# Kernel tuning notes

Hardware: AMD Instinct MI355X
Metric: run time of the kernel (lower is better)

## Reference

```python
import jax, jax.numpy as jnp
import numpy as np

B, N, D_IN, D_OUT = 64, 307, 64, 64
ALPHA = 0.2  # LeakyReLU negative slope
NEG_INF = -9e15


def _build_adj(n, seed=0):
    # Mimic the module's constant adjacency buffer structure:
    # 2n x 2n, bottom-right = A, top-left = A, top-right = I, bottom-left = 0.
    rng = np.random.RandomState(seed)
    A = (rng.rand(n, n) < 0.05).astype(np.float32)
    np.fill_diagonal(A, 1.0)
    full = np.zeros((2 * n, 2 * n), dtype=np.float32)
    full[n:, n:] = A
    full[:n, :n] = A
    full[:n, n:] = np.eye(n, dtype=np.float32)
    return jnp.asarray(full)


def setup_inputs() -> dict:
    key = jax.random.key(0)
    k1, k2, k3, k4 = jax.random.split(key, 4)
    h = jax.random.normal(k1, (B, N, D_IN), dtype=jnp.float32)
    ht = jax.random.normal(k2, (B, N, D_IN), dtype=jnp.float32)
    # xavier_uniform-ish params
    bw = 1.414 * np.sqrt(6.0 / (D_IN + D_OUT))
    W = jax.random.uniform(k3, (D_IN, D_OUT), dtype=jnp.float32, minval=-bw, maxval=bw)
    ba = 1.414 * np.sqrt(6.0 / (2 * D_OUT + 1))
    a = jax.random.uniform(k4, (2 * D_OUT, 1), dtype=jnp.float32, minval=-ba, maxval=ba)
    adj = _build_adj(N)
    return {"h": h, "ht": ht, "W": W, "a": a, "adj": adj}


def reference(h, ht, W, a, adj):
    n = N
    x = jnp.concatenate([ht, h], axis=1)          # [b, 2n, d_in]
    Wh = jnp.einsum('bni,io->bno', x, W)          # [b, 2n, d_out]
    Wh1 = Wh @ a[:D_OUT]                          # [b, 2n, 1]
    Wh2 = Wh @ a[D_OUT:]                          # [b, 2n, 1]
    e = jax.nn.leaky_relu(Wh1 + jnp.swapaxes(Wh2, 1, 2), negative_slope=ALPHA)  # [b,2n,2n]
    att = jnp.where(adj > 0, e, NEG_INF)
    att = jax.nn.softmax(att, axis=1)             # NOTE: softmax over dim=1 as in source
    # dropout is identity in eval mode (training=False)
    h_prime = jnp.einsum('bnm,bmo->bno', att, Wh)  # [b, 2n, d_out]
    h_prime = jnp.concatenate([h_prime[:, :n], h_prime[:, n:]], axis=-1)  # [b, n, 2*d_out]
    return jax.nn.elu(h_prime)
```

## Files before the change

### kernel.cpp

```cpp
#include <hip/hip_runtime.h>
#include <hip/hip_bf16.h>
#include <math.h>

#define NB   64
#define NN   307
#define MM   614
#define DD   64
#define CAP  64
#define LRA  0.2f
#define WHB  39
#define NTASK (NB * NN)

__device__ __forceinline__ float wave_sum(float v) {
  #pragma unroll
  for (int m = 32; m >= 1; m >>= 1) v += __shfl_xor(v, m);
  return v;
}
__device__ __forceinline__ float lrelu(float v) { return v > 0.f ? v : LRA * v; }

__global__ __launch_bounds__(256) void k_prep(const float* __restrict__ h,
    const float* __restrict__ ht, const float* __restrict__ W,
    const float* __restrict__ a, const float* __restrict__ adj,
    int* __restrict__ arow_cnt, int* __restrict__ arow_idx,
    int* __restrict__ acol_cnt, int* __restrict__ acol_idx,
    float* __restrict__ Wh, float* __restrict__ Wh1, float* __restrict__ Wh2) {
  int tid = threadIdx.x;
  int bid = blockIdx.x;

  if (bid < 2 * NN) {
    __shared__ int cnt;
    if (tid == 0) cnt = 0;
    __syncthreads();
    if (bid < NN) {
      int r = bid;
      for (int j = tid; j < NN; j += 256)
        if (adj[(size_t)r * MM + j] > 0.f)
          arow_idx[r * CAP + atomicAdd(&cnt, 1)] = j;
      __syncthreads();
      if (tid == 0) arow_cnt[r] = cnt;
    } else {
      int c = bid - NN;
      for (int i = tid; i < NN; i += 256)
        if (adj[(size_t)i * MM + c] > 0.f)
          acol_idx[c * CAP + atomicAdd(&cnt, 1)] = i;
      __syncthreads();
      if (tid == 0) acol_cnt[c] = cnt;
    }
    return;
  }

  __shared__ float Wl[DD * DD];
  __shared__ float xst[4][DD][4];
  #pragma unroll
  for (int k = 0; k < 16; k++) Wl[tid + k * 256] = W[tid + k * 256];

  int lane = tid & 63;
  int wv   = __builtin_amdgcn_readfirstlane(tid >> 6);
  int blk  = bid - 2 * NN;
  int b    = blk / WHB;
  int r0   = (blk % WHB) * 16 + wv * 4;

  const float* xp[4];
  bool valid[4];
  #pragma unroll
  for (int j = 0; j < 4; j++) {
    int r = r0 + j;
    valid[j] = (r < MM);
    int rc = valid[j] ? r : 0;
    xp[j] = (rc < NN) ? (ht + ((size_t)b * NN + rc) * DD)
                      : (h  + ((size_t)b * NN + (rc - NN)) * DD);
  }
  int jr = lane & 3, el = lane >> 2;
  #pragma unroll
  for (int t = 0; t < 4; t++) {
    float v = xp[jr][t * 16 + el];
    xst[wv][t * 16 + el][jr] = v;
  }
  __syncthreads();

  float a1 = a[lane], a2 = a[64 + lane];
  float acc0 = 0.f, acc1 = 0.f, acc2 = 0.f, acc3 = 0.f;
  #pragma unroll
  for (int i = 0; i < 64; i++) {
    float4 xv = *(const float4*)&xst[wv][i][0];
    float w = Wl[i * 64 + lane];
    acc0 = fmaf(xv.x, w, acc0);
    acc1 = fmaf(xv.y, w, acc1);
    acc2 = fmaf(xv.z, w, acc2);
    acc3 = fmaf(xv.w, w, acc3);
  }

  float accs[4] = {acc0, acc1, acc2, acc3};
  #pragma unroll
  for (int j = 0; j < 4; j++) {
    float p1 = wave_sum(accs[j] * a1);
    float p2 = wave_sum(accs[j] * a2);
    int r = r0 + j;
    if (valid[j]) {
      Wh[((size_t)(b * MM + r)) * DD + lane] = accs[j];
      if (lane == 0) { Wh1[b * MM + r] = p1; Wh2[b * MM + r] = p2; }
    }
  }
}

__global__ __launch_bounds__(256) void k_stats(const float* __restrict__ Wh1,
    const float* __restrict__ Wh2, const int* __restrict__ acol_cnt,
    const int* __restrict__ acol_idx, float4* __restrict__ stats) {
  int lane = threadIdx.x & 63;
  int task = blockIdx.x * 4 + (threadIdx.x >> 6);
  int b = task / NN, j = task - b * NN;
  const float* wh1 = Wh1 + (size_t)b * MM;
  float wh2j  = Wh2[(size_t)b * MM + j];
  float wh2nj = Wh2[(size_t)b * MM + NN + j];
  int cnt = acol_cnt[j];
  float s0 = 0.f, s1 = 0.f;
  if (lane < cnt) {
    int i = acol_idx[j * CAP + lane];
    s0 = __expf(lrelu(wh1[i] + wh2j));
    s1 = __expf(lrelu(wh1[NN + i] + wh2nj));
  }
  s0 = wave_sum(s0);
  s1 = wave_sum(s1);
  s1 += __expf(lrelu(wh1[j] + wh2nj));
  if (lane == 0) stats[task] = make_float4(wh2j, wh2nj, 1.f / s0, 1.f / s1);
}

__global__ __launch_bounds__(256) void k_out(const float* __restrict__ Wh,
    const float* __restrict__ Wh1, const float4* __restrict__ stats,
    const int* __restrict__ arow_cnt, const int* __restrict__ arow_idx,
    float* __restrict__ out) {
  int lane = threadIdx.x & 63;
  int bid = blockIdx.x;
  int sb = (bid & 7) * 614 + (bid >> 3);
  int task = sb * 4 + (threadIdx.x >> 6);
  int b = task / NN, i = task - b * NN;
  const float* whB = Wh + (size_t)b * MM * DD;
  float wh1a = Wh1[(size_t)b * MM + i];
  float wh1b = Wh1[(size_t)b * MM + NN + i];
  int rcnt = arow_cnt[i];
  int j = 0;
  float w0 = 0.f, w1 = 0.f;
  if (lane < rcnt) {
    j = arow_idx[i * CAP + lane];
    float4 st = stats[(size_t)b * NN + j];
    w0 = __expf(lrelu(wh1a + st.x)) * st.z;
    w1 = __expf(lrelu(wh1b + st.y)) * st.w;
  }
  float acc0a = 0.f, acc0b = 0.f, acc1a = 0.f, acc1b = 0.f;
  for (int k = 0; k + 1 < rcnt; k += 2) {
    int   jka = __shfl(j, k),   jkb = __shfl(j, k + 1);
    float w0a = __shfl(w0, k),  w0b = __shfl(w0, k + 1);
    float w1a = __shfl(w1, k),  w1b = __shfl(w1, k + 1);
    const float* pa = whB + (size_t)jka * DD + lane;
    const float* pb = whB + (size_t)jkb * DD + lane;
    acc0a = fmaf(w0a, pa[0], acc0a);
    acc1a = fmaf(w1a, pa[NN * DD], acc1a);
    acc0b = fmaf(w0b, pb[0], acc0b);
    acc1b = fmaf(w1b, pb[NN * DD], acc1b);
  }
  if (rcnt & 1) {
    int k = rcnt - 1;
    int   jka = __shfl(j, k);
    float w0a = __shfl(w0, k), w1a = __shfl(w1, k);
    const float* pa = whB + (size_t)jka * DD + lane;
    acc0a = fmaf(w0a, pa[0], acc0a);
    acc1a = fmaf(w1a, pa[NN * DD], acc1a);
  }
  float4 sti = stats[(size_t)b * NN + i];
  acc0a = fmaf(__expf(lrelu(wh1a + sti.y)) * sti.w,
               whB[(size_t)(NN + i) * DD + lane], acc0a);
  float acc0 = acc0a + acc0b, acc1 = acc1a + acc1b;
  float r0 = acc0 > 0.f ? acc0 : expm1f(acc0);
  float r1 = acc1 > 0.f ? acc1 : expm1f(acc1);
  out[((size_t)(b * NN + i)) * 128 + lane]      = r0;
  out[((size_t)(b * NN + i)) * 128 + 64 + lane] = r1;
}

extern "C" void kernel_launch(void* const* d_in, const int* in_sizes, int n_in,
                              void* d_out, int out_size, void* d_ws, size_t ws_size,
                              hipStream_t stream) {
  const float* h   = (const float*)d_in[0];
  const float* ht  = (const float*)d_in[1];
  const float* W   = (const float*)d_in[2];
  const float* a   = (const float*)d_in[3];
  const float* adj = (const float*)d_in[4];
  float* out = (float*)d_out;

  char* ws = (char*)d_ws;
  size_t off = 0;
  auto alloc = [&](size_t bytes) -> void* {
    void* p = ws + off;
    off = (off + bytes + 255) & ~(size_t)255;
    return p;
  };
  float*  Wh       = (float*)alloc((size_t)NB * MM * DD * 4);
  float4* stats    = (float4*)alloc((size_t)NB * NN * 16);
  float*  Wh1      = (float*)alloc((size_t)NB * MM * 4);
  float*  Wh2      = (float*)alloc((size_t)NB * MM * 4);
  int*    arow_cnt = (int*)alloc(NN * 4);
  int*    acol_cnt = (int*)alloc(NN * 4);
  int*    arow_idx = (int*)alloc((size_t)NN * CAP * 4);
  int*    acol_idx = (int*)alloc((size_t)NN * CAP * 4);

  k_prep<<<2 * NN + NB * WHB, 256, 0, stream>>>(h, ht, W, a, adj,
      arow_cnt, arow_idx, acol_cnt, acol_idx, Wh, Wh1, Wh2);
  k_stats<<<NTASK / 4, 256, 0, stream>>>(Wh1, Wh2, acol_cnt, acol_idx, stats);
  k_out<<<NTASK / 4, 256, 0, stream>>>(Wh, Wh1, stats, arow_cnt, arow_idx, out);
}
```

Before: 138.9 us.

## Fuse projection, softmax stats and aggregation into one per-batch kernel with LDS-resident Wh

Splits out the adjacency index build into its own kernel. The Wh projection, column softmax statistics and sparse aggregation are merged into a single kernel with one 1024-thread block per batch. Wh (stored as bf16), Wh1, Wh2 and the stats live in shared memory, so the global round trips for these intermediates and two launches go away. The cost is that only 64 blocks run, leaving most CUs idle, and bf16 storage of Wh reduces precision.

Result: slower. 206.8 us (+48.8%).

```diff
diff --git a/kernel.cpp b/kernel.cpp
--- a/kernel.cpp
+++ b/kernel.cpp
@@ -8,8 +8,6 @@
 #define DD   64
 #define CAP  64
 #define LRA  0.2f
-#define WHB  39
-#define NTASK (NB * NN)
 
 __device__ __forceinline__ float wave_sum(float v) {
   #pragma unroll
@@ -18,162 +16,143 @@
 }
 __device__ __forceinline__ float lrelu(float v) { return v > 0.f ? v : LRA * v; }
 
-__global__ __launch_bounds__(256) void k_prep(const float* __restrict__ h,
-    const float* __restrict__ ht, const float* __restrict__ W,
-    const float* __restrict__ a, const float* __restrict__ adj,
+__global__ __launch_bounds__(256) void k_adj(const float* __restrict__ adj,
     int* __restrict__ arow_cnt, int* __restrict__ arow_idx,
-    int* __restrict__ acol_cnt, int* __restrict__ acol_idx,
-    float* __restrict__ Wh, float* __restrict__ Wh1, float* __restrict__ Wh2) {
+    int* __restrict__ acol_cnt, int* __restrict__ acol_idx) {
   int tid = threadIdx.x;
   int bid = blockIdx.x;
+  __shared__ int cnt;
+  if (tid == 0) cnt = 0;
+  __syncthreads();
+  if (bid < NN) {
+    int r = bid;
+    for (int j = tid; j < NN; j += 256)
+      if (adj[(size_t)r * MM + j] > 0.f)
+        arow_idx[r * CAP + atomicAdd(&cnt, 1)] = j;
+    __syncthreads();
+    if (tid == 0) arow_cnt[r] = cnt;
+  } else {
+    int c = bid - NN;
+    for (int i = tid; i < NN; i += 256)
+      if (adj[(size_t)i * MM + c] > 0.f)
+        acol_idx[c * CAP + atomicAdd(&cnt, 1)] = i;
+    __syncthreads();
+    if (tid == 0) acol_cnt[c] = cnt;
+  }
+}
 
-  if (bid < 2 * NN) {
-    __shared__ int cnt;
-    if (tid == 0) cnt = 0;
-    __syncthreads();
-    if (bid < NN) {
-      int r = bid;
-      for (int j = tid; j < NN; j += 256)
-        if (adj[(size_t)r * MM + j] > 0.f)
-          arow_idx[r * CAP + atomicAdd(&cnt, 1)] = j;
-      __syncthreads();
-      if (tid == 0) arow_cnt[r] = cnt;
-    } else {
-      int c = bid - NN;
-      for (int i = tid; i < NN; i += 256)
-        if (adj[(size_t)i * MM + c] > 0.f)
-          acol_idx[c * CAP + atomicAdd(&cnt, 1)] = i;
-      __syncthreads();
-      if (tid == 0) acol_cnt[c] = cnt;
+__global__ __launch_bounds__(1024, 1) void k_batch(
+    const float* __restrict__ h, const float* __restrict__ ht,
+    const float* __restrict__ W, const float* __restrict__ a,
+    const int* __restrict__ arow_cnt, const int* __restrict__ arow_idx,
+    const int* __restrict__ acol_cnt, const int* __restrict__ acol_idx,
+    float* __restrict__ out) {
+  __shared__ float          Wl[DD * DD];
+  __shared__ __hip_bfloat16 Whl[MM * DD];
+  __shared__ float          Wh1l[MM];
+  __shared__ float          Wh2l[MM];
+  __shared__ float4         statsl[NN];
+
+  const int tid  = threadIdx.x;
+  const int b    = blockIdx.x;
+  const int lane = tid & 63;
+  const int wv   = __builtin_amdgcn_readfirstlane(tid >> 6);
+
+  reinterpret_cast<float4*>(Wl)[tid] = reinterpret_cast<const float4*>(W)[tid];
+  __syncthreads();
+
+  const float a1 = a[lane], a2 = a[64 + lane];
+
+  for (int p = 0; p < 10; p++) {
+    int r0 = p * 64 + wv * 4;
+    const float* xp[4];
+    bool valid[4];
+    #pragma unroll
+    for (int j = 0; j < 4; j++) {
+      int r = r0 + j;
+      valid[j] = (r < MM);
+      int rc = valid[j] ? r : 0;
+      xp[j] = (rc < NN) ? (ht + ((size_t)b * NN + rc) * DD)
+                        : (h  + ((size_t)b * NN + (rc - NN)) * DD);
     }
-    return;
-  }
-
-  __shared__ float Wl[DD * DD];
-  __shared__ float xst[4][DD][4];
-  #pragma unroll
-  for (int k = 0; k < 16; k++) Wl[tid + k * 256] = W[tid + k * 256];
-
-  int lane = tid & 63;
-  int wv   = __builtin_amdgcn_readfirstlane(tid >> 6);
-  int blk  = bid - 2 * NN;
-  int b    = blk / WHB;
-  int r0   = (blk % WHB) * 16 + wv * 4;
-
-  const float* xp[4];
-  bool valid[4];
-  #pragma unroll
-  for (int j = 0; j < 4; j++) {
-    int r = r0 + j;
-    valid[j] = (r < MM);
-    int rc = valid[j] ? r : 0;
-    xp[j] = (rc < NN) ? (ht + ((size_t)b * NN + rc) * DD)
-                      : (h  + ((size_t)b * NN + (rc - NN)) * DD);
-  }
-  int jr = lane & 3, el = lane >> 2;
-  #pragma unroll
-  for (int t = 0; t < 4; t++) {
-    float v = xp[jr][t * 16 + el];
-    xst[wv][t * 16 + el][jr] = v;
+    float acc0 = 0.f, acc1 = 0.f, acc2 = 0.f, acc3 = 0.f;
+    #pragma unroll
+    for (int i = 0; i < 64; i++) {
+      float w = Wl[i * 64 + lane];
+      acc0 = fmaf(xp[0][i], w, acc0);
+      acc1 = fmaf(xp[1][i], w, acc1);
+      acc2 = fmaf(xp[2][i], w, acc2);
+      acc3 = fmaf(xp[3][i], w, acc3);
+    }
+    float accs[4] = {acc0, acc1, acc2, acc3};
+    #pragma unroll
+    for (int j = 0; j < 4; j++) {
+      float p1 = wave_sum(accs[j] * a1);
+      float p2 = wave_sum(accs[j] * a2);
+      int r = r0 + j;
+      if (valid[j]) {
+        Whl[r * 64 + lane] = __float2bfloat16(accs[j]);
+        if (lane == 0) { Wh1l[r] = p1; Wh2l[r] = p2; }
+      }
+    }
   }
   __syncthreads();
 
-  float a1 = a[lane], a2 = a[64 + lane];
-  float acc0 = 0.f, acc1 = 0.f, acc2 = 0.f, acc3 = 0.f;
-  #pragma unroll
-  for (int i = 0; i < 64; i++) {
-    float4 xv = *(const float4*)&xst[wv][i][0];
-    float w = Wl[i * 64 + lane];
-    acc0 = fmaf(xv.x, w, acc0);
-    acc1 = fmaf(xv.y, w, acc1);
-    acc2 = fmaf(xv.z, w, acc2);
-    acc3 = fmaf(xv.w, w, acc3);
+  for (int j = wv; j < NN; j += 16) {
+    int cnt = acol_cnt[j];
+    float wh2j  = Wh2l[j];
+    float wh2nj = Wh2l[NN + j];
+    float s0 = 0.f, s1 = 0.f;
+    if (lane < cnt) {
+      int i = acol_idx[j * CAP + lane];
+      s0 = __expf(lrelu(Wh1l[i] + wh2j));
+      s1 = __expf(lrelu(Wh1l[NN + i] + wh2nj));
+    }
+    s0 = wave_sum(s0);
+    s1 = wave_sum(s1);
+    s1 += __expf(lrelu(Wh1l[j] + wh2nj));
+    if (lane == 0) statsl[j] = make_float4(wh2j, wh2nj, 1.f / s0, 1.f / s1);
   }
+  __syncthreads();
 
-  float accs[4] = {acc0, acc1, acc2, acc3};
-  #pragma unroll
-  for (int j = 0; j < 4; j++) {
-    float p1 = wave_sum(accs[j] * a1);
-    float p2 = wave_sum(accs[j] * a2);
-    int r = r0 + j;
-    if (valid[j]) {
-      Wh[((size_t)(b * MM + r)) * DD + lane] = accs[j];
-      if (lane == 0) { Wh1[b * MM + r] = p1; Wh2[b * MM + r] = p2; }
+  for (int i = wv; i < NN; i += 16) {
+    int rcnt = arow_cnt[i];
+    float wh1a = Wh1l[i];
+    float wh1b = Wh1l[NN + i];
+    int j = 0;
+    float w0 = 0.f, w1 = 0.f;
+    if (lane < rcnt) {
+      j = arow_idx[i * CAP + lane];
+      float4 st = statsl[j];
+      w0 = __expf(lrelu(wh1a + st.x)) * st.z;
+      w1 = __expf(lrelu(wh1b + st.y)) * st.w;
     }
+    float acc0a = 0.f, acc0b = 0.f, acc1a = 0.f, acc1b = 0.f;
+    for (int k = 0; k + 1 < rcnt; k += 2) {
+      int   jka = __shfl(j, k),   jkb = __shfl(j, k + 1);
+      float w0a = __shfl(w0, k),  w0b = __shfl(w0, k + 1);
+      float w1a = __shfl(w1, k),  w1b = __shfl(w1, k + 1);
+      acc0a = fmaf(w0a, __bfloat162float(Whl[jka * 64 + lane]), acc0a);
+      acc1a = fmaf(w1a, __bfloat162float(Whl[(NN + jka) * 64 + lane]), acc1a);
+      acc0b = fmaf(w0b, __bfloat162float(Whl[jkb * 64 + lane]), acc0b);
+      acc1b = fmaf(w1b, __bfloat162float(Whl[(NN + jkb) * 64 + lane]), acc1b);
+    }
+    if (rcnt & 1) {
+      int k = rcnt - 1;
+      int   jka = __shfl(j, k);
+      float w0a = __shfl(w0, k), w1a = __shfl(w1, k);
+      acc0a = fmaf(w0a, __bfloat162float(Whl[jka * 64 + lane]), acc0a);
+      acc1a = fmaf(w1a, __bfloat162float(Whl[(NN + jka) * 64 + lane]), acc1a);
+    }
+    float4 sti = statsl[i];
+    acc0a = fmaf(__expf(lrelu(wh1a + sti.y)) * sti.w,
+                 __bfloat162float(Whl[(NN + i) * 64 + lane]), acc0a);
+    float acc0 = acc0a + acc0b, acc1 = acc1a + acc1b;
+    float r0 = acc0 > 0.f ? acc0 : expm1f(acc0);
+    float r1 = acc1 > 0.f ? acc1 : expm1f(acc1);
+    out[((size_t)(b * NN + i)) * 128 + lane]      = r0;
+    out[((size_t)(b * NN + i)) * 128 + 64 + lane] = r1;
   }
-}
-
-__global__ __launch_bounds__(256) void k_stats(const float* __restrict__ Wh1,
-    const float* __restrict__ Wh2, const int* __restrict__ acol_cnt,
-    const int* __restrict__ acol_idx, float4* __restrict__ stats) {
-  int lane = threadIdx.x & 63;
-  int task = blockIdx.x * 4 + (threadIdx.x >> 6);
-  int b = task / NN, j = task - b * NN;
-  const float* wh1 = Wh1 + (size_t)b * MM;
-  float wh2j  = Wh2[(size_t)b * MM + j];
-  float wh2nj = Wh2[(size_t)b * MM + NN + j];
-  int cnt = acol_cnt[j];
-  float s0 = 0.f, s1 = 0.f;
-  if (lane < cnt) {
-    int i = acol_idx[j * CAP + lane];
-    s0 = __expf(lrelu(wh1[i] + wh2j));
-    s1 = __expf(lrelu(wh1[NN + i] + wh2nj));
-  }
-  s0 = wave_sum(s0);
-  s1 = wave_sum(s1);
-  s1 += __expf(lrelu(wh1[j] + wh2nj));
-  if (lane == 0) stats[task] = make_float4(wh2j, wh2nj, 1.f / s0, 1.f / s1);
-}
-
-__global__ __launch_bounds__(256) void k_out(const float* __restrict__ Wh,
-    const float* __restrict__ Wh1, const float4* __restrict__ stats,
-    const int* __restrict__ arow_cnt, const int* __restrict__ arow_idx,
-    float* __restrict__ out) {
-  int lane = threadIdx.x & 63;
-  int bid = blockIdx.x;
-  int sb = (bid & 7) * 614 + (bid >> 3);
-  int task = sb * 4 + (threadIdx.x >> 6);
-  int b = task / NN, i = task - b * NN;
-  const float* whB = Wh + (size_t)b * MM * DD;
-  float wh1a = Wh1[(size_t)b * MM + i];
-  float wh1b = Wh1[(size_t)b * MM + NN + i];
-  int rcnt = arow_cnt[i];
-  int j = 0;
-  float w0 = 0.f, w1 = 0.f;
-  if (lane < rcnt) {
-    j = arow_idx[i * CAP + lane];
-    float4 st = stats[(size_t)b * NN + j];
-    w0 = __expf(lrelu(wh1a + st.x)) * st.z;
-    w1 = __expf(lrelu(wh1b + st.y)) * st.w;
-  }
-  float acc0a = 0.f, acc0b = 0.f, acc1a = 0.f, acc1b = 0.f;
-  for (int k = 0; k + 1 < rcnt; k += 2) {
-    int   jka = __shfl(j, k),   jkb = __shfl(j, k + 1);
-    float w0a = __shfl(w0, k),  w0b = __shfl(w0, k + 1);
-    float w1a = __shfl(w1, k),  w1b = __shfl(w1, k + 1);
-    const float* pa = whB + (size_t)jka * DD + lane;
-    const float* pb = whB + (size_t)jkb * DD + lane;
-    acc0a = fmaf(w0a, pa[0], acc0a);
-    acc1a = fmaf(w1a, pa[NN * DD], acc1a);
-    acc0b = fmaf(w0b, pb[0], acc0b);
-    acc1b = fmaf(w1b, pb[NN * DD], acc1b);
-  }
-  if (rcnt & 1) {
-    int k = rcnt - 1;
-    int   jka = __shfl(j, k);
-    float w0a = __shfl(w0, k), w1a = __shfl(w1, k);
-    const float* pa = whB + (size_t)jka * DD + lane;
-    acc0a = fmaf(w0a, pa[0], acc0a);
-    acc1a = fmaf(w1a, pa[NN * DD], acc1a);
-  }
-  float4 sti = stats[(size_t)b * NN + i];
-  acc0a = fmaf(__expf(lrelu(wh1a + sti.y)) * sti.w,
-               whB[(size_t)(NN + i) * DD + lane], acc0a);
-  float acc0 = acc0a + acc0b, acc1 = acc1a + acc1b;
-  float r0 = acc0 > 0.f ? acc0 : expm1f(acc0);
-  float r1 = acc1 > 0.f ? acc1 : expm1f(acc1);
-  out[((size_t)(b * NN + i)) * 128 + lane]      = r0;
-  out[((size_t)(b * NN + i)) * 128 + 64 + lane] = r1;
 }
 
 extern "C" void kernel_launch(void* const* d_in, const int* in_sizes, int n_in,
@@ -193,17 +172,12 @@
     off = (off + bytes + 255) & ~(size_t)255;
     return p;
   };
-  float*  Wh       = (float*)alloc((size_t)NB * MM * DD * 4);
-  float4* stats    = (float4*)alloc((size_t)NB * NN * 16);
-  float*  Wh1      = (float*)alloc((size_t)NB * MM * 4);
-  float*  Wh2      = (float*)alloc((size_t)NB * MM * 4);
-  int*    arow_cnt = (int*)alloc(NN * 4);
-  int*    acol_cnt = (int*)alloc(NN * 4);
-  int*    arow_idx = (int*)alloc((size_t)NN * CAP * 4);
-  int*    acol_idx = (int*)alloc((size_t)NN * CAP * 4);
+  int* arow_cnt = (int*)alloc(NN * 4);
+  int* acol_cnt = (int*)alloc(NN * 4);
+  int* arow_idx = (int*)alloc((size_t)NN * CAP * 4);
+  int* acol_idx = (int*)alloc((size_t)NN * CAP * 4);
 
-  k_prep<<<2 * NN + NB * WHB, 256, 0, stream>>>(h, ht, W, a, adj,
-      arow_cnt, arow_idx, acol_cnt, acol_idx, Wh, Wh1, Wh2);
-  k_stats<<<NTASK / 4, 256, 0, stream>>>(Wh1, Wh2, acol_cnt, acol_idx, stats);
-  k_out<<<NTASK / 4, 256, 0, stream>>>(Wh, Wh1, stats, arow_cnt, arow_idx, out);
+  k_adj<<<2 * NN, 256, 0, stream>>>(adj, arow_cnt, arow_idx, acol_cnt, acol_idx);
+  k_batch<<<NB, 1024, 0, stream>>>(h, ht, W, a,
+      arow_cnt, arow_idx, acol_cnt, acol_idx, out);
 }
```
